# Optimization experiments

Measured on AMD Instinct MI355X. Metric: run time of the kernel, lower is better.

Reference implementation:

```python
import jax, jax.numpy as jnp
import numpy as np

BATCH, IN_DIM, HID_DIM, OUT_DIM, K = 8192, 256, 16384, 256, 256


def setup_inputs() -> dict:
    key = jax.random.key(0)
    k1, k2, k3 = jax.random.split(key, 3)
    x = jax.random.normal(k1, (BATCH, IN_DIM), dtype=jnp.float32)
    # kaiming_uniform-like init scale for encoder/decoder weights
    enc_w = jax.random.normal(k2, (HID_DIM, IN_DIM), dtype=jnp.float32) * (1.0 / np.sqrt(IN_DIM))
    enc_b = jnp.zeros((HID_DIM,), dtype=jnp.float32)
    dec_w = jax.random.normal(k3, (OUT_DIM, HID_DIM), dtype=jnp.float32) * (1.0 / np.sqrt(HID_DIM))
    dec_b = jnp.zeros((OUT_DIM,), dtype=jnp.float32)
    return {"x": x, "enc_w": enc_w, "enc_b": enc_b, "dec_w": dec_w, "dec_b": dec_b, "k": K}


def reference(x, enc_w, enc_b, dec_w, dec_b, k):
    # encoder: [B, in] @ [in, hid] -> [B, hid]
    hidden_pre = x @ enc_w.T + enc_b
    h_relu = jax.nn.relu(hidden_pre)
    kk = min(h_relu.shape[1], int(k))
    # k-th largest value per row as threshold; mask = (x_relu >= threshold)
    topk_vals, _ = jax.lax.top_k(h_relu, kk)          # [B, k]
    thresholds = topk_vals[:, -1:]                    # [B, 1]
    hidden_post = jnp.where(h_relu >= thresholds, h_relu, 0.0)
    # decoder: [B, hid] @ [hid, out] -> [B, out]
    output = hidden_post @ dec_w.T + dec_b
    return (output, hidden_post)
```

## Files before the change

### kernel.cpp

```cpp
#include <hip/hip_runtime.h>
#include <stdint.h>

#define BATCH   8192
#define IN_DIM  256
#define HID_DIM 16384
#define OUT_DIM 256

#define SELCAPF 2048

typedef __attribute__((ext_vector_type(4))) float f32x4;

__device__ __forceinline__ float bf16u_to_f(unsigned short u) {
  return __uint_as_float(((unsigned)u) << 16);
}
__device__ __forceinline__ unsigned short f_to_bf16_rne(float f) {
  unsigned u = __float_as_uint(f);
  u += 0x7fffu + ((u >> 16) & 1u);
  return (unsigned short)(u >> 16);
}
__device__ __forceinline__ int read_k(const int* kptr) {
  int k = kptr[0];
  if (k <= 0 || k > 100000000) {
    float kf = __int_as_float(k);
    if (kf >= 1.f && kf <= 16384.f) k = (int)kf;
  }
  if (k < 1) k = 1;
  if (k > HID_DIM) k = HID_DIM;
  return k;
}

__global__ __launch_bounds__(256) void k_transb(const float* __restrict__ dec_w,
                                                unsigned short* __restrict__ decT) {
  __shared__ float tile[32][33];
  int j0 = blockIdx.x * 32, o0 = blockIdx.y * 32;
  int tx = threadIdx.x & 31, ty = threadIdx.x >> 5;
#pragma unroll
  for (int rr = 0; rr < 4; rr++)
    tile[ty + rr * 8][tx] = dec_w[(size_t)(o0 + ty + rr * 8) * HID_DIM + (j0 + tx)];
  __syncthreads();
#pragma unroll
  for (int rr = 0; rr < 4; rr++)
    decT[(size_t)(j0 + ty + rr * 8) * OUT_DIM + (o0 + tx)] = f_to_bf16_rne(tile[tx][ty + rr * 8]);
}

__global__ __launch_bounds__(256, 2) void k_gemm1f2(const float* __restrict__ X,
                                                    const float* __restrict__ W,
                                                    const float* __restrict__ encb,
                                                    float* __restrict__ hid) {
  __shared__ float As[64][132];
  __shared__ float Bs[64][132];
  const int bn = blockIdx.x, bm = blockIdx.y;
  const int t = threadIdx.x;
  const int tx = t & 15, ty = t >> 4;
  const int sr = t >> 1, sh = t & 1;

  float acc[8][8] = {};

  const float* Ab = X + (size_t)(bm * 128) * IN_DIM;
  const float* Bb = W + (size_t)(bn * 128) * IN_DIM;

  for (int k0 = 0; k0 < IN_DIM; k0 += 64) {
#pragma unroll
    for (int j = 0; j < 8; j++) {
      const int ko = sh * 32 + j * 4;
      const float4 av = *(const float4*)&Ab[(size_t)sr * IN_DIM + k0 + ko];
      As[ko + 0][sr] = av.x; As[ko + 1][sr] = av.y;
      As[ko + 2][sr] = av.z; As[ko + 3][sr] = av.w;
      const float4 bv = *(const float4*)&Bb[(size_t)sr * IN_DIM + k0 + ko];
      Bs[ko + 0][sr] = bv.x; Bs[ko + 1][sr] = bv.y;
      Bs[ko + 2][sr] = bv.z; Bs[ko + 3][sr] = bv.w;
    }
    __syncthreads();
#pragma unroll 4
    for (int kk = 0; kk < 64; kk++) {
      float a[8], b[8];
      *(float4*)&a[0] = *(const float4*)&As[kk][ty * 8];
      *(float4*)&a[4] = *(const float4*)&As[kk][ty * 8 + 4];
      *(float4*)&b[0] = *(const float4*)&Bs[kk][tx * 8];
      *(float4*)&b[4] = *(const float4*)&Bs[kk][tx * 8 + 4];
#pragma unroll
      for (int i = 0; i < 8; i++)
#pragma unroll
        for (int j = 0; j < 8; j++)
          acc[i][j] = fmaf(a[i], b[j], acc[i][j]);
    }
    __syncthreads();
  }

#pragma unroll
  for (int i = 0; i < 8; i++) {
    const int m = bm * 128 + ty * 8 + i;
    float4 o1, o2;
    float* p1 = (float*)&o1;
    float* p2 = (float*)&o2;
#pragma unroll
    for (int j = 0; j < 4; j++) {
      const float h = acc[i][j] + encb[bn * 128 + tx * 8 + j];
      p1[j] = (h > 0.f) ? h : 0.f;
    }
#pragma unroll
    for (int j = 0; j < 4; j++) {
      const float h = acc[i][4 + j] + encb[bn * 128 + tx * 8 + 4 + j];
      p2[j] = (h > 0.f) ? h : 0.f;
    }
    float* dst = &hid[(size_t)m * HID_DIM + bn * 128 + tx * 8];
    *(float4*)dst = o1;
    *(float4*)(dst + 4) = o2;
  }
}

__global__ __launch_bounds__(256) void k_topk3(const unsigned short* __restrict__ decTb,
                                               const float* __restrict__ decb,
                                               const int* __restrict__ kptr,
                                               float* __restrict__ out,
                                               float* __restrict__ hid) {
  __shared__ unsigned hist[8][257];
  __shared__ unsigned cums[257];
  __shared__ float selV[SELCAPF];
  __shared__ unsigned short selI[SELCAPF];
  __shared__ unsigned s_selcnt, s_b, s_need;
  __shared__ int s_keepall;

  const int r = blockIdx.x, t = threadIdx.x;
  float* hrow = hid + (size_t)r * HID_DIM;
  const int k = read_k(kptr);

  f32x4 row[16];
#pragma unroll
  for (int c = 0; c < 16; c++) row[c] = *(const f32x4*)&hrow[(c * 256 + t) * 4];

  for (int i = t; i < 8 * 257; i += 256) ((unsigned*)hist)[i] = 0u;
  if (t == 0) { s_selcnt = 0; s_keepall = 0; }
  __syncthreads();

#pragma unroll
  for (int c = 0; c < 16; c++)
#pragma unroll
    for (int e = 0; e < 4; e++) {
      const unsigned b = __float_as_uint(row[c][e]) >> 24;
      if (b) atomicAdd(&hist[t & 7][b], 1u);
    }
  __syncthreads();
  { unsigned s = 0;
#pragma unroll
    for (int cpy = 0; cpy < 8; cpy++) s += hist[cpy][t];
    cums[t] = s; }
  __syncthreads();
  for (int off = 1; off < 256; off <<= 1) {
    const unsigned v = cums[t];
    const unsigned a = (t + off < 256) ? cums[t + off] : 0u;
    __syncthreads();
    cums[t] = v + a;
    __syncthreads();
  }
  if (t == 0 && cums[1] < (unsigned)k) s_keepall = 1;
  if (t >= 1) {
    const unsigned incl = cums[t], excl = (t < 255) ? cums[t + 1] : 0u;
    if (incl >= (unsigned)k && excl < (unsigned)k) { s_b = (unsigned)t; s_need = (unsigned)k - excl; }
  }
  __syncthreads();

  unsigned prefix = 0;
  const int keepall = s_keepall;
  if (!keepall) {
    prefix = s_b << 24;
    unsigned need = s_need;
    for (int pass = 0; pass < 3; pass++) {
      const int shift = 16 - pass * 8;
      for (int i = t; i < 8 * 257; i += 256) ((unsigned*)hist)[i] = 0u;
      __syncthreads();
      const unsigned pfx = prefix;
      const int pshift = shift + 8;
#pragma unroll
      for (int c = 0; c < 16; c++)
#pragma unroll
        for (int e = 0; e < 4; e++) {
          const unsigned bits = __float_as_uint(row[c][e]);
          if ((bits >> pshift) == (pfx >> pshift))
            atomicAdd(&hist[t & 7][(bits >> shift) & 255u], 1u);
        }
      __syncthreads();
      { unsigned s = 0;
#pragma unroll
        for (int cpy = 0; cpy < 8; cpy++) s += hist[cpy][t];
        cums[t] = s; }
      __syncthreads();
      for (int off = 1; off < 256; off <<= 1) {
        const unsigned v = cums[t];
        const unsigned a = (t + off < 256) ? cums[t + off] : 0u;
        __syncthreads();
        cums[t] = v + a;
        __syncthreads();
      }
      { const unsigned incl = cums[t], excl = (t < 255) ? cums[t + 1] : 0u;
        if (incl >= need && excl < need) { s_b = (unsigned)t; s_need = need - excl; } }
      __syncthreads();
      prefix |= s_b << shift;
      need = s_need;
      __syncthreads();
    }
  }
  const unsigned T = prefix;

#pragma unroll
  for (int c = 0; c < 16; c++) {
    const int base = (c * 256 + t) * 4;
    f32x4 o;
#pragma unroll
    for (int e = 0; e < 4; e++) {
      const float v = row[c][e];
      const unsigned bits = __float_as_uint(v);
      const bool keep = keepall || (bits >= T);
      o[e] = keep ? v : 0.f;
      if (keep && bits != 0u) {
        const unsigned p = atomicAdd(&s_selcnt, 1u);
        if (p < SELCAPF) { selV[p] = v; selI[p] = (unsigned short)(base + e); }
      }
    }
    *(f32x4*)&hrow[base] = o;
  }
  __syncthreads();

  const unsigned nsel = s_selcnt;
  float a0 = decb[t], a1 = 0.f, a2 = 0.f, a3 = 0.f;
  if (nsel <= SELCAPF) {
    unsigned s = 0;
    for (; s + 4 <= nsel; s += 4) {
      a0 += selV[s + 0] * bf16u_to_f(decTb[(size_t)selI[s + 0] * OUT_DIM + t]);
      a1 += selV[s + 1] * bf16u_to_f(decTb[(size_t)selI[s + 1] * OUT_DIM + t]);
      a2 += selV[s + 2] * bf16u_to_f(decTb[(size_t)selI[s + 2] * OUT_DIM + t]);
      a3 += selV[s + 3] * bf16u_to_f(decTb[(size_t)selI[s + 3] * OUT_DIM + t]);
    }
    for (; s < nsel; s++)
      a0 += selV[s] * bf16u_to_f(decTb[(size_t)selI[s] * OUT_DIM + t]);
  } else {
    for (int j = 0; j < HID_DIM; j++) {
      const float hv = hrow[j];
      if (hv != 0.f) a0 += hv * bf16u_to_f(decTb[(size_t)j * OUT_DIM + t]);
    }
  }
  out[(size_t)r * OUT_DIM + t] = (a0 + a1) + (a2 + a3);
}

__global__ __launch_bounds__(256) void k_topkf(const float* __restrict__ dec,
                                               const float* __restrict__ decb,
                                               const int* __restrict__ kptr,
                                               float* __restrict__ out,
                                               float* __restrict__ hid) {
  __shared__ unsigned hist[8][257];
  __shared__ unsigned tot[256];
  __shared__ float selV[SELCAPF];
  __shared__ unsigned short selI[SELCAPF];
  __shared__ unsigned s_selcnt, s_need, s_pref, s_byte;
  __shared__ int s_keepall;

  const int r = blockIdx.x, t = threadIdx.x;
  float* hrow = hid + (size_t)r * HID_DIM;
  const int k = read_k(kptr);

  for (int i = t; i < 8 * 257; i += 256) ((unsigned*)hist)[i] = 0u;
  if (t == 0) { s_selcnt = 0; s_keepall = 0; s_pref = 0; }
  __syncthreads();
#pragma unroll
  for (int c = 0; c < 16; c++) {
    const f32x4 v = *(const f32x4*)&hrow[(c * 256 + t) * 4];
#pragma unroll
    for (int e = 0; e < 4; e++) {
      const unsigned b = __float_as_uint(v[e]) >> 24;
      if (b) atomicAdd(&hist[t & 7][b], 1u);
    }
  }
  __syncthreads();
  { unsigned s = 0;
#pragma unroll
    for (int c = 0; c < 8; c++) s += hist[c][t];
    tot[t] = s; }
  __syncthreads();
  if (t == 0) {
    unsigned cum = 0; int b1 = -1; unsigned need = 0;
    for (int b = 255; b >= 1; b--) {
      const unsigned c = tot[b];
      if (cum + c >= (unsigned)k) { b1 = b; need = (unsigned)k - cum; break; }
      cum += c;
    }
    if (b1 < 0) s_keepall = 1;
    else { s_pref = ((unsigned)b1) << 24; s_need = need; }
  }
  __syncthreads();
  if (!s_keepall) {
    for (int pass = 1; pass <= 3; pass++) {
      const int shift = 24 - pass * 8;
      tot[t] = 0;
      __syncthreads();
      const unsigned prefhi = s_pref >> (shift + 8);
#pragma unroll
      for (int c = 0; c < 16; c++) {
        const f32x4 v = *(const f32x4*)&hrow[(c * 256 + t) * 4];
#pragma unroll
        for (int e = 0; e < 4; e++) {
          const unsigned bits = __float_as_uint(v[e]);
          if ((bits >> (shift + 8)) == prefhi) atomicAdd(&tot[(bits >> shift) & 255u], 1u);
        }
      }
      __syncthreads();
      if (t == 0) {
        unsigned cum = 0; const unsigned need = s_need;
        for (int b = 255; b >= 0; b--) {
          const unsigned c = tot[b];
          if (cum + c >= need) { s_byte = (unsigned)b; s_need = need - cum; break; }
          cum += c;
        }
        s_pref |= s_byte << shift;
      }
      __syncthreads();
    }
  }
  const int keepall = s_keepall;
  const unsigned T = s_pref;
#pragma unroll
  for (int c = 0; c < 16; c++) {
    const int base = (c * 256 + t) * 4;
    const f32x4 v = *(const f32x4*)&hrow[base];
    f32x4 o;
#pragma unroll
    for (int e = 0; e < 4; e++) {
      const unsigned bits = __float_as_uint(v[e]);
      const bool keep = keepall || (bits >= T);
      o[e] = keep ? v[e] : 0.f;
      if (keep && bits != 0u) {
        const unsigned p = atomicAdd(&s_selcnt, 1u);
        if (p < SELCAPF) { selV[p] = v[e]; selI[p] = (unsigned short)(base + e); }
      }
    }
    *(f32x4*)&hrow[base] = o;
  }
  __syncthreads();
  const unsigned nsel = s_selcnt;
  float a0 = decb[t], a1 = 0.f, a2 = 0.f, a3 = 0.f;
  if (nsel <= SELCAPF) {
    unsigned s = 0;
    for (; s + 4 <= nsel; s += 4) {
#pragma unroll
      for (int u = 0; u < 4; u++) {
        const unsigned idx = selI[s + u];
        const float wv = dec[(size_t)t * HID_DIM + idx];
        (u == 0 ? a0 : u == 1 ? a1 : u == 2 ? a2 : a3) += selV[s + u] * wv;
      }
    }
    for (; s < nsel; s++)
      a0 += selV[s] * dec[(size_t)t * HID_DIM + selI[s]];
  } else {
    for (int j = 0; j < HID_DIM; j++) {
      const float hv = hrow[j];
      if (hv != 0.f) a0 += hv * dec[(size_t)t * HID_DIM + j];
    }
  }
  out[(size_t)r * OUT_DIM + t] = (a0 + a1) + (a2 + a3);
}

extern "C" void kernel_launch(void* const* d_in, const int* in_sizes, int n_in,
                              void* d_out, int out_size, void* d_ws, size_t ws_size,
                              hipStream_t stream) {
  int ix = 0, iew = 1, ieb = 2, idw = 3, idb = 4, ik = 5;
  if (n_in >= 6 && in_sizes[0] == OUT_DIM && in_sizes[5] == BATCH * IN_DIM) {
    idb = 0; idw = 1; ieb = 2; iew = 3; ik = 4; ix = 5;
  }
  const float* x     = (const float*)d_in[ix];
  const float* enc_w = (const float*)d_in[iew];
  const float* enc_b = (const float*)d_in[ieb];
  const float* dec_w = (const float*)d_in[idw];
  const float* dec_b = (const float*)d_in[idb];
  const int*   kptr  = (const int*)d_in[ik];

  float* out = (float*)d_out;
  float* hid = out + (size_t)BATCH * OUT_DIM;

  k_gemm1f2<<<dim3(HID_DIM / 128, BATCH / 128), 256, 0, stream>>>(x, enc_w, enc_b, hid);

  const size_t B_decT = (size_t)HID_DIM * OUT_DIM * 2;
  if (ws_size >= 64 + B_decT) {
    unsigned short* decTb = (unsigned short*)((char*)d_ws + 64);
    k_transb<<<dim3(HID_DIM / 32, OUT_DIM / 32), 256, 0, stream>>>(dec_w, decTb);
    k_topk3<<<dim3(BATCH), 256, 0, stream>>>(decTb, dec_b, kptr, out, hid);
  } else {
    k_topkf<<<dim3(BATCH), 256, 0, stream>>>(dec_w, dec_b, kptr, out, hid);
  }
}
```

Baseline: 1.612 ms.

## Use packed FMA encoder GEMM and candidate-based radix top-k selection

The encoder GEMM now uses packed two-wide FMA on float2 accumulators, with a 32-deep K tile and a launch bound of 4 blocks per SM. The top-k threshold search replaces four 8-bit radix passes with a single 4096-bin histogram over the top 13 bits. Elements in the selected bin are gathered as candidates and ranked by brute-force comparison, with 4-bit refinement passes only if that bin holds too many. The aim is to cut FMA instruction count and the barriers and atomics of the multi-pass radix select, at the cost of a single-copy histogram (more atomic contention) and an O(n^2) candidate rank.

```diff
diff --git a/kernel.cpp b/kernel.cpp
--- a/kernel.cpp
+++ b/kernel.cpp
@@ -7,8 +7,11 @@
 #define OUT_DIM 256
 
 #define SELCAPF 2048
+#define TKBINS  4096
+#define TKCAND  512
 
 typedef __attribute__((ext_vector_type(4))) float f32x4;
+typedef __attribute__((ext_vector_type(2))) float f32x2;
 
 __device__ __forceinline__ float bf16u_to_f(unsigned short u) {
   return __uint_as_float(((unsigned)u) << 16);
@@ -28,6 +31,13 @@
   if (k > HID_DIM) k = HID_DIM;
   return k;
 }
+__device__ __forceinline__ f32x2 fma2(f32x2 a, f32x2 b, f32x2 c) {
+#if __has_builtin(__builtin_elementwise_fma)
+  return __builtin_elementwise_fma(a, b, c);
+#else
+  f32x2 r; r[0] = fmaf(a[0], b[0], c[0]); r[1] = fmaf(a[1], b[1], c[1]); return r;
+#endif
+}
 
 __global__ __launch_bounds__(256) void k_transb(const float* __restrict__ dec_w,
                                                 unsigned short* __restrict__ decT) {
@@ -43,26 +53,26 @@
     decT[(size_t)(j0 + ty + rr * 8) * OUT_DIM + (o0 + tx)] = f_to_bf16_rne(tile[tx][ty + rr * 8]);
 }
 
-__global__ __launch_bounds__(256, 2) void k_gemm1f2(const float* __restrict__ X,
+__global__ __launch_bounds__(256, 4) void k_gemm_pk(const float* __restrict__ X,
                                                     const float* __restrict__ W,
                                                     const float* __restrict__ encb,
                                                     float* __restrict__ hid) {
-  __shared__ float As[64][132];
-  __shared__ float Bs[64][132];
+  __shared__ float As[32][132];
+  __shared__ float Bs[32][132];
   const int bn = blockIdx.x, bm = blockIdx.y;
   const int t = threadIdx.x;
   const int tx = t & 15, ty = t >> 4;
-  const int sr = t >> 1, sh = t & 1;
-
-  float acc[8][8] = {};
+  const int sr = t & 127, sh = t >> 7;
+
+  f32x2 acc[8][4] = {};
 
   const float* Ab = X + (size_t)(bm * 128) * IN_DIM;
   const float* Bb = W + (size_t)(bn * 128) * IN_DIM;
 
-  for (int k0 = 0; k0 < IN_DIM; k0 += 64) {
-#pragma unroll
-    for (int j = 0; j < 8; j++) {
-      const int ko = sh * 32 + j * 4;
+  for (int k0 = 0; k0 < IN_DIM; k0 += 32) {
+#pragma unroll
+    for (int q = 0; q < 4; q++) {
+      const int ko = sh * 16 + q * 4;
       const float4 av = *(const float4*)&Ab[(size_t)sr * IN_DIM + k0 + ko];
       As[ko + 0][sr] = av.x; As[ko + 1][sr] = av.y;
       As[ko + 2][sr] = av.z; As[ko + 3][sr] = av.w;
@@ -71,18 +81,22 @@
       Bs[ko + 2][sr] = bv.z; Bs[ko + 3][sr] = bv.w;
     }
     __syncthreads();
-#pragma unroll 4
-    for (int kk = 0; kk < 64; kk++) {
-      float a[8], b[8];
+#pragma unroll 8
+    for (int kk = 0; kk < 32; kk++) {
+      float a[8]; f32x2 b2[4];
       *(float4*)&a[0] = *(const float4*)&As[kk][ty * 8];
       *(float4*)&a[4] = *(const float4*)&As[kk][ty * 8 + 4];
-      *(float4*)&b[0] = *(const float4*)&Bs[kk][tx * 8];
-      *(float4*)&b[4] = *(const float4*)&Bs[kk][tx * 8 + 4];
-#pragma unroll
-      for (int i = 0; i < 8; i++)
-#pragma unroll
-        for (int j = 0; j < 8; j++)
-          acc[i][j] = fmaf(a[i], b[j], acc[i][j]);
+      const float4 b0 = *(const float4*)&Bs[kk][tx * 8];
+      const float4 b1 = *(const float4*)&Bs[kk][tx * 8 + 4];
+      b2[0][0] = b0.x; b2[0][1] = b0.y; b2[1][0] = b0.z; b2[1][1] = b0.w;
+      b2[2][0] = b1.x; b2[2][1] = b1.y; b2[3][0] = b1.z; b2[3][1] = b1.w;
+#pragma unroll
+      for (int i = 0; i < 8; i++) {
+        f32x2 ai; ai[0] = a[i]; ai[1] = a[i];
+#pragma unroll
+        for (int j = 0; j < 4; j++)
+          acc[i][j] = fma2(ai, b2[j], acc[i][j]);
+      }
     }
     __syncthreads();
   }
@@ -90,35 +104,32 @@
 #pragma unroll
   for (int i = 0; i < 8; i++) {
     const int m = bm * 128 + ty * 8 + i;
-    float4 o1, o2;
-    float* p1 = (float*)&o1;
-    float* p2 = (float*)&o2;
+    float o[8];
 #pragma unroll
     for (int j = 0; j < 4; j++) {
-      const float h = acc[i][j] + encb[bn * 128 + tx * 8 + j];
-      p1[j] = (h > 0.f) ? h : 0.f;
-    }
-#pragma unroll
-    for (int j = 0; j < 4; j++) {
-      const float h = acc[i][4 + j] + encb[bn * 128 + tx * 8 + 4 + j];
-      p2[j] = (h > 0.f) ? h : 0.f;
+      const float h0 = acc[i][j][0] + encb[bn * 128 + tx * 8 + j * 2];
+      const float h1 = acc[i][j][1] + encb[bn * 128 + tx * 8 + j * 2 + 1];
+      o[j * 2]     = (h0 > 0.f) ? h0 : 0.f;
+      o[j * 2 + 1] = (h1 > 0.f) ? h1 : 0.f;
     }
     float* dst = &hid[(size_t)m * HID_DIM + bn * 128 + tx * 8];
-    *(float4*)dst = o1;
-    *(float4*)(dst + 4) = o2;
-  }
-}
-
-__global__ __launch_bounds__(256) void k_topk3(const unsigned short* __restrict__ decTb,
+    *(float4*)dst = *(float4*)&o[0];
+    *(float4*)(dst + 4) = *(float4*)&o[4];
+  }
+}
+
+__global__ __launch_bounds__(256) void k_topk4(const unsigned short* __restrict__ decTb,
                                                const float* __restrict__ decb,
                                                const int* __restrict__ kptr,
                                                float* __restrict__ out,
                                                float* __restrict__ hid) {
-  __shared__ unsigned hist[8][257];
-  __shared__ unsigned cums[257];
+  __shared__ unsigned hist[TKBINS];
+  __shared__ unsigned part[257];
+  __shared__ unsigned candB[TKCAND];
+  __shared__ unsigned short candI[TKCAND];
   __shared__ float selV[SELCAPF];
   __shared__ unsigned short selI[SELCAPF];
-  __shared__ unsigned s_selcnt, s_b, s_need;
+  __shared__ unsigned s_selcnt, s_cnt, s_T, s_need, s_bin;
   __shared__ int s_keepall;
 
   const int r = blockIdx.x, t = threadIdx.x;
@@ -129,78 +140,110 @@
 #pragma unroll
   for (int c = 0; c < 16; c++) row[c] = *(const f32x4*)&hrow[(c * 256 + t) * 4];
 
-  for (int i = t; i < 8 * 257; i += 256) ((unsigned*)hist)[i] = 0u;
-  if (t == 0) { s_selcnt = 0; s_keepall = 0; }
+  for (int i = t; i < TKBINS; i += 256) hist[i] = 0u;
+  if (t == 0) { s_selcnt = 0; s_cnt = 0; s_keepall = 0; s_T = 0; }
   __syncthreads();
 
 #pragma unroll
   for (int c = 0; c < 16; c++)
 #pragma unroll
     for (int e = 0; e < 4; e++) {
-      const unsigned b = __float_as_uint(row[c][e]) >> 24;
-      if (b) atomicAdd(&hist[t & 7][b], 1u);
-    }
-  __syncthreads();
-  { unsigned s = 0;
-#pragma unroll
-    for (int cpy = 0; cpy < 8; cpy++) s += hist[cpy][t];
-    cums[t] = s; }
+      const unsigned bin = __float_as_uint(row[c][e]) >> 19;
+      if (bin) atomicAdd(&hist[bin], 1u);
+    }
+  __syncthreads();
+
+  { unsigned s = 0; const int b0 = t * 16;
+#pragma unroll
+    for (int u = 0; u < 16; u++) s += hist[b0 + u];
+    part[t] = s; }
   __syncthreads();
   for (int off = 1; off < 256; off <<= 1) {
-    const unsigned v = cums[t];
-    const unsigned a = (t + off < 256) ? cums[t + off] : 0u;
+    const unsigned v = part[t];
+    const unsigned a = (t + off < 256) ? part[t + off] : 0u;
     __syncthreads();
-    cums[t] = v + a;
+    part[t] = v + a;
     __syncthreads();
   }
-  if (t == 0 && cums[1] < (unsigned)k) s_keepall = 1;
-  if (t >= 1) {
-    const unsigned incl = cums[t], excl = (t < 255) ? cums[t + 1] : 0u;
-    if (incl >= (unsigned)k && excl < (unsigned)k) { s_b = (unsigned)t; s_need = (unsigned)k - excl; }
-  }
-  __syncthreads();
-
-  unsigned prefix = 0;
+  if (t == 0 && part[0] < (unsigned)k) s_keepall = 1;
+  {
+    const unsigned incl = part[t], excl = (t < 255) ? part[t + 1] : 0u;
+    if (incl >= (unsigned)k && excl < (unsigned)k) {
+      unsigned cum = excl; int bin = t * 16; unsigned need = 1;
+      for (int b = t * 16 + 15; b >= t * 16; b--) {
+        const unsigned c2 = hist[b];
+        if (cum + c2 >= (unsigned)k) { bin = b; need = (unsigned)k - cum; break; }
+        cum += c2;
+      }
+      s_bin = (unsigned)bin; s_need = need;
+    }
+  }
+  __syncthreads();
+
   const int keepall = s_keepall;
+  unsigned T = 0u;
   if (!keepall) {
-    prefix = s_b << 24;
-    unsigned need = s_need;
-    for (int pass = 0; pass < 3; pass++) {
-      const int shift = 16 - pass * 8;
-      for (int i = t; i < 8 * 257; i += 256) ((unsigned*)hist)[i] = 0u;
-      __syncthreads();
-      const unsigned pfx = prefix;
-      const int pshift = shift + 8;
+    int shift = 19;
+    unsigned prefix = s_bin;
+    for (;;) {
+      if (t == 0) s_cnt = 0;
+      __syncthreads();
 #pragma unroll
       for (int c = 0; c < 16; c++)
 #pragma unroll
         for (int e = 0; e < 4; e++) {
           const unsigned bits = __float_as_uint(row[c][e]);
-          if ((bits >> pshift) == (pfx >> pshift))
-            atomicAdd(&hist[t & 7][(bits >> shift) & 255u], 1u);
-        }
-      __syncthreads();
-      { unsigned s = 0;
-#pragma unroll
-        for (int cpy = 0; cpy < 8; cpy++) s += hist[cpy][t];
-        cums[t] = s; }
-      __syncthreads();
-      for (int off = 1; off < 256; off <<= 1) {
-        const unsigned v = cums[t];
-        const unsigned a = (t + off < 256) ? cums[t + off] : 0u;
-        __syncthreads();
-        cums[t] = v + a;
-        __syncthreads();
-      }
-      { const unsigned incl = cums[t], excl = (t < 255) ? cums[t + 1] : 0u;
-        if (incl >= need && excl < need) { s_b = (unsigned)t; s_need = need - excl; } }
-      __syncthreads();
-      prefix |= s_b << shift;
-      need = s_need;
-      __syncthreads();
-    }
-  }
-  const unsigned T = prefix;
+          if ((bits >> shift) == prefix) {
+            const unsigned p = atomicAdd(&s_cnt, 1u);
+            if (p < TKCAND) { candB[p] = bits; candI[p] = (unsigned short)((c * 256 + t) * 4 + e); }
+          }
+        }
+      __syncthreads();
+      if (s_cnt <= TKCAND || shift == 0) break;
+      const int nsh = (shift >= 4) ? shift - 4 : 0;
+      const int nb = shift - nsh;
+      if (t < (1 << nb)) part[t] = 0u;
+      __syncthreads();
+#pragma unroll
+      for (int c = 0; c < 16; c++)
+#pragma unroll
+        for (int e = 0; e < 4; e++) {
+          const unsigned bits = __float_as_uint(row[c][e]);
+          if ((bits >> shift) == prefix)
+            atomicAdd(&part[(bits >> nsh) & ((1u << nb) - 1u)], 1u);
+        }
+      __syncthreads();
+      if (t == 0) {
+        unsigned cum = 0; const unsigned need = s_need;
+        for (int b = (1 << nb) - 1; b >= 0; b--) {
+          const unsigned c2 = part[b];
+          if (cum + c2 >= need) { s_bin = (unsigned)b; s_need = need - cum; break; }
+          cum += c2;
+        }
+      }
+      __syncthreads();
+      prefix = (prefix << nb) | s_bin;
+      shift = nsh;
+      __syncthreads();
+    }
+    if (shift == 0) {
+      if (t == 0) s_T = prefix;
+    } else {
+      const unsigned n = s_cnt;
+      const unsigned need = s_need;
+      for (unsigned i = t; i < n; i += 256) {
+        const unsigned v = candB[i];
+        unsigned g = 0, e = 0;
+        for (unsigned j = 0; j < n; j++) {
+          const unsigned u = candB[j];
+          g += (u > v); e += (u == v);
+        }
+        if (g < need && need <= g + e) s_T = v;
+      }
+    }
+    __syncthreads();
+    T = s_T;
+  }
 
 #pragma unroll
   for (int c = 0; c < 16; c++) {
@@ -343,8 +386,7 @@
 #pragma unroll
       for (int u = 0; u < 4; u++) {
         const unsigned idx = selI[s + u];
-        const float wv = dec[(size_t)t * HID_DIM + idx];
-        (u == 0 ? a0 : u == 1 ? a1 : u == 2 ? a2 : a3) += selV[s + u] * wv;
+        (u == 0 ? a0 : u == 1 ? a1 : u == 2 ? a2 : a3) += selV[s + u] * dec[(size_t)t * HID_DIM + idx];
       }
     }
     for (; s < nsel; s++)
@@ -375,13 +417,13 @@
   float* out = (float*)d_out;
   float* hid = out + (size_t)BATCH * OUT_DIM;
 
-  k_gemm1f2<<<dim3(HID_DIM / 128, BATCH / 128), 256, 0, stream>>>(x, enc_w, enc_b, hid);
+  k_gemm_pk<<<dim3(HID_DIM / 128, BATCH / 128), 256, 0, stream>>>(x, enc_w, enc_b, hid);
 
   const size_t B_decT = (size_t)HID_DIM * OUT_DIM * 2;
   if (ws_size >= 64 + B_decT) {
     unsigned short* decTb = (unsigned short*)((char*)d_ws + 64);
     k_transb<<<dim3(HID_DIM / 32, OUT_DIM / 32), 256, 0, stream>>>(dec_w, decTb);
-    k_topk3<<<dim3(BATCH), 256, 0, stream>>>(decTb, dec_b, kptr, out, hid);
+    k_topk4<<<dim3(BATCH), 256, 0, stream>>>(decTb, dec_b, kptr, out, hid);
   } else {
     k_topkf<<<dim3(BATCH), 256, 0, stream>>>(dec_w, dec_b, kptr, out, hid);
   }
```

After: 1.599 ms. No clear change (-0.8%).
